# Kernel optimization log

Hardware: AMD Instinct MI355X
Metric: run time of the kernel (lower is better)

Reference implementation:

```python
import jax, jax.numpy as jnp
import numpy as np

D = 1024      # model dimension
H = 16        # heads
DK = D // H   # head dim
DFF = 4096    # ffn hidden
B, S = 2, 2048
EPS = 1e-6
NEG_SLOPE = 0.01  # torch LeakyReLU default


def setup_inputs() -> dict:
    key = jax.random.key(0)
    ks = jax.random.split(key, 12)
    sd = 1.0 / np.sqrt(D)
    sf = 1.0 / np.sqrt(DFF)
    return {
        "x": jax.random.normal(ks[0], (B, S, D), dtype=jnp.float32),
        "wq": jax.random.uniform(ks[1], (D, D), jnp.float32, -sd, sd),
        "bq": jnp.zeros((D,), jnp.float32),
        "wk": jax.random.uniform(ks[2], (D, D), jnp.float32, -sd, sd),
        "bk": jnp.zeros((D,), jnp.float32),
        "wv": jax.random.uniform(ks[3], (D, D), jnp.float32, -sd, sd),
        "bv": jnp.zeros((D,), jnp.float32),
        "wo": jax.random.uniform(ks[4], (D, D), jnp.float32, -sd, sd),
        "bo": jnp.zeros((D,), jnp.float32),
        "g1": jnp.ones((D,), jnp.float32),
        "b1": jnp.zeros((D,), jnp.float32),
        "w_ff1": jax.random.uniform(ks[5], (D, DFF), jnp.float32, -sd, sd),
        "b_ff1": jnp.zeros((DFF,), jnp.float32),
        "w_ff2": jax.random.uniform(ks[6], (DFF, D), jnp.float32, -sf, sf),
        "b_ff2": jnp.zeros((D,), jnp.float32),
        "g2": jnp.ones((D,), jnp.float32),
        "b2": jnp.zeros((D,), jnp.float32),
    }


def _layernorm(x, g, b):
    mu = jnp.mean(x, axis=-1, keepdims=True)
    var = jnp.mean(jnp.square(x - mu), axis=-1, keepdims=True)
    return (x - mu) * jax.lax.rsqrt(var + EPS) * g + b


def reference(x, wq, bq, wk, bk, wv, bv, wo, bo, g1, b1,
              w_ff1, b_ff1, w_ff2, b_ff2, g2, b2):
    # Multi-head attention
    q = (x @ wq + bq).reshape(B, S, H, DK).transpose(0, 2, 1, 3)  # [B,H,S,DK]
    k = (x @ wk + bk).reshape(B, S, H, DK).transpose(0, 2, 1, 3)
    v = (x @ wv + bv).reshape(B, S, H, DK).transpose(0, 2, 1, 3)
    scores = jnp.einsum('bhqd,bhkd->bhqk', q, k) / np.sqrt(DK)
    attn = jax.nn.softmax(scores, axis=-1)
    ctx = jnp.einsum('bhqk,bhkd->bhqd', attn, v)
    ctx = ctx.transpose(0, 2, 1, 3).reshape(B, S, D)
    attn_out = ctx @ wo + bo
    # residual + LN1 (dropout = identity in eval)
    h = _layernorm(attn_out + x, g1, b1)
    # FFN with LeakyReLU
    ff = jnp.where(h @ w_ff1 + b_ff1 > 0,
                   h @ w_ff1 + b_ff1,
                   NEG_SLOPE * (h @ w_ff1 + b_ff1))
    ff = ff @ w_ff2 + b_ff2
    return _layernorm(ff + h, g2, b2)
```

## Files before the change

### kernel.cpp

```cpp
#include <hip/hip_runtime.h>
#include <math.h>

#define D_MODEL 1024
#define NHEAD   16
#define DKH     64
#define DFF_    4096
#define BB      2
#define SS      2048
#define MTOT    (BB*SS)
#define EPSLN   1e-6f
#define NEG_SLOPE 0.01f

typedef unsigned short u16;
typedef unsigned int   u32;
typedef __bf16 bf16x8 __attribute__((ext_vector_type(8)));
typedef float  f32x4  __attribute__((ext_vector_type(4)));
typedef u16    u16x4  __attribute__((ext_vector_type(4)));

__device__ __forceinline__ u16 f2bf(float f) {
    u32 u = __float_as_uint(f);
    u = (u + 0x7fffu + ((u >> 16) & 1u)) >> 16;
    return (u16)u;
}
__device__ __forceinline__ float bf2f(u16 u) {
    return __uint_as_float(((u32)u) << 16);
}

__device__ __forceinline__ void gload_lds16(const u16* g, u16* l) {
    __builtin_amdgcn_global_load_lds(
        (const __attribute__((address_space(1))) u32*)g,
        (__attribute__((address_space(3))) u32*)l,
        16, 0, 0);
}

__device__ __forceinline__ void transpose_tile(const float* __restrict__ W,
        u16* __restrict__ WT, int N, int out_stride, int out_row_off,
        float scale, int bx, int by, u16* T)
{
    const int t  = threadIdx.x;
    const int n0 = bx * 64;
    const int k0 = by * 64;
    #pragma unroll
    for (int i = 0; i < 4; ++i) {
        int r = i * 16 + (t >> 4);
        int c = (t & 15) * 4;
        float4 v = *(const float4*)&W[(size_t)(k0 + r) * N + n0 + c];
        T[(c + 0) * 72 + r] = f2bf(v.x * scale);
        T[(c + 1) * 72 + r] = f2bf(v.y * scale);
        T[(c + 2) * 72 + r] = f2bf(v.z * scale);
        T[(c + 3) * 72 + r] = f2bf(v.w * scale);
    }
    __syncthreads();
    #pragma unroll
    for (int i = 0; i < 4; ++i) {
        int nr = i * 16 + (t >> 4);
        int kc = (t & 15) * 4;
        u16x4 o = { T[nr*72 + kc], T[nr*72 + kc + 1], T[nr*72 + kc + 2], T[nr*72 + kc + 3] };
        *(u16x4*)&WT[(size_t)(out_row_off + n0 + nr) * out_stride + k0 + kc] = o;
    }
}

__global__ __launch_bounds__(256)
void prep(const float* __restrict__ x, u16* __restrict__ x_bf,
          const float* __restrict__ wq, const float* __restrict__ wk,
          const float* __restrict__ wv, const float* __restrict__ wo,
          const float* __restrict__ wff1, const float* __restrict__ wff2,
          u16* __restrict__ wqkvT, u16* __restrict__ woT,
          u16* __restrict__ wff1T, u16* __restrict__ wff2T,
          const float* __restrict__ bq, const float* __restrict__ bk,
          const float* __restrict__ bv, float* __restrict__ qkv_bias,
          float qscale)
{
    __shared__ u16 T[64 * 72];
    int blk = blockIdx.x;
    if (blk < 4096) {
        int i = blk * 256 + threadIdx.x;
        float4 v = ((const float4*)x)[i];
        u16x4 o = { f2bf(v.x), f2bf(v.y), f2bf(v.z), f2bf(v.w) };
        ((u16x4*)x_bf)[i] = o;
        return;
    }
    blk -= 4096;
    if (blk < 1024) {
        int which = blk >> 8, r = blk & 255;
        const float* Ws = which == 0 ? wq : which == 1 ? wk : which == 2 ? wv : wo;
        u16* Wd   = which == 3 ? woT : wqkvT;
        int off   = which == 3 ? 0 : which * 1024;
        float sc  = which == 0 ? qscale : 1.0f;
        transpose_tile(Ws, Wd, 1024, 1024, off, sc, r & 15, r >> 4, T);
        return;
    }
    blk -= 1024;
    if (blk < 1024) {
        transpose_tile(wff1, wff1T, 4096, 1024, 0, 1.0f, blk & 63, blk >> 6, T);
        return;
    }
    blk -= 1024;
    if (blk < 1024) {
        transpose_tile(wff2, wff2T, 1024, 4096, 0, 1.0f, blk & 15, blk >> 4, T);
        return;
    }
    blk -= 1024;
    int i = blk * 256 + threadIdx.x;
    qkv_bias[i] = (i < 1024) ? bq[i] * qscale
                : (i < 2048) ? bk[i - 1024] : bv[i - 2048];
}

template<int EPI>
__global__ __launch_bounds__(256)
void gemm_bf16(const u16* __restrict__ A, const u16* __restrict__ BT,
               const float* __restrict__ bias, void* __restrict__ Cout,
               u16* __restrict__ Vt, int M, int N, int k_len, int kstride)
{
    __shared__ u16 As[128 * 64];
    __shared__ u16 Bs[128 * 64];
    const int tid  = threadIdx.x;
    const int w    = tid >> 6;
    const int lane = tid & 63;
    const int lm   = lane & 15;
    const int lq   = lane >> 4;
    const int nf = gridDim.x * gridDim.y;
    int f = blockIdx.y * gridDim.x + blockIdx.x;
    f = (f & 7) * (nf >> 3) + (f >> 3);
    const int row0 = (f / gridDim.x) * 128;
    const int col0 = (f % gridDim.x) * 128;
    const int k_off = blockIdx.z * k_len;
    const int wrow = (w >> 1) * 64;
    const int wcol = (w & 1) * 64;

    f32x4 acc[4][4] = {};

    const int r_i = lane >> 3;
    const int csw = ((lane & 7) ^ r_i) * 8;
    const u16* a_src = A  + (size_t)(row0 + w * 32 + r_i) * kstride + k_off + csw;
    const u16* b_src = BT + (size_t)(col0 + w * 32 + r_i) * kstride + k_off + csw;
    u16* a_dst = &As[(w * 32) * 64];
    u16* b_dst = &Bs[(w * 32) * 64];

    const int fr0 = (lq ^ (lm & 7)) * 8;
    const int fr1 = ((4 + lq) ^ (lm & 7)) * 8;
    const u16* a_rd = &As[(wrow + lm) * 64];
    const u16* b_rd = &Bs[(wcol + lm) * 64];

    for (int k0 = 0; k0 < k_len; k0 += 64) {
        #pragma unroll
        for (int i = 0; i < 4; ++i) {
            gload_lds16(a_src + k0 + (size_t)(i * 8) * kstride, a_dst + (i * 8) * 64);
            gload_lds16(b_src + k0 + (size_t)(i * 8) * kstride, b_dst + (i * 8) * 64);
        }
        __syncthreads();
        #pragma unroll
        for (int h = 0; h < 2; ++h) {
            const int fo = h ? fr1 : fr0;
            bf16x8 av[4], bv[4];
            #pragma unroll
            for (int m = 0; m < 4; ++m) av[m] = *(const bf16x8*)(a_rd + m * 16 * 64 + fo);
            #pragma unroll
            for (int n = 0; n < 4; ++n) bv[n] = *(const bf16x8*)(b_rd + n * 16 * 64 + fo);
            #pragma unroll
            for (int m = 0; m < 4; ++m)
                #pragma unroll
                for (int n = 0; n < 4; ++n)
                    acc[m][n] = __builtin_amdgcn_mfma_f32_16x16x32_bf16(av[m], bv[n], acc[m][n], 0, 0, 0);
        }
        __syncthreads();
    }

    float bz[4] = {0.f, 0.f, 0.f, 0.f};
    if (EPI != 3) {
        #pragma unroll
        for (int n = 0; n < 4; ++n) bz[n] = bias[col0 + wcol + n * 16 + lm];
    }

    u16* Cz = (u16*)Cout + (EPI == 3 ? (size_t)blockIdx.z * M * N : 0);
    #pragma unroll
    for (int m = 0; m < 4; ++m) {
        #pragma unroll
        for (int e = 0; e < 4; ++e) {
            int row = row0 + wrow + m * 16 + lq * 4 + e;
            #pragma unroll
            for (int n = 0; n < 4; ++n) {
                int col = col0 + wcol + n * 16 + lm;
                float v = acc[m][n][e] + bz[n];
                if (EPI == 1) v = v > 0.f ? v : NEG_SLOPE * v;
                Cz[(size_t)row * N + col] = f2bf(v);
            }
        }
    }
}

#define GPHASE(p) { \
    bf16x8 a0h0 = *(const bf16x8*)&ar[(wm * 128 + (p) * 32 + lm) * 64 + fr0]; \
    bf16x8 a0h1 = *(const bf16x8*)&ar[(wm * 128 + (p) * 32 + lm) * 64 + fr1]; \
    bf16x8 a1h0 = *(const bf16x8*)&ar[(wm * 128 + (p) * 32 + 16 + lm) * 64 + fr0]; \
    bf16x8 a1h1 = *(const bf16x8*)&ar[(wm * 128 + (p) * 32 + 16 + lm) * 64 + fr1]; \
    _Pragma("unroll") \
    for (int n = 0; n < 4; ++n) { \
        acc[2*(p)][n]   = __builtin_amdgcn_mfma_f32_16x16x32_bf16(a0h0, bvf[n][0], acc[2*(p)][n], 0, 0, 0); \
        acc[2*(p)][n]   = __builtin_amdgcn_mfma_f32_16x16x32_bf16(a0h1, bvf[n][1], acc[2*(p)][n], 0, 0, 0); \
        acc[2*(p)+1][n] = __builtin_amdgcn_mfma_f32_16x16x32_bf16(a1h0, bvf[n][0], acc[2*(p)+1][n], 0, 0, 0); \
        acc[2*(p)+1][n] = __builtin_amdgcn_mfma_f32_16x16x32_bf16(a1h1, bvf[n][1], acc[2*(p)+1][n], 0, 0, 0); \
    } }

template<int EPI>
__global__ __launch_bounds__(512, 2)
void gemm256(const u16* __restrict__ A, const u16* __restrict__ BT,
             const float* __restrict__ bias, void* __restrict__ Cout,
             u16* __restrict__ Vt, int M, int N, int k_len, int kstride)
{
    __shared__ u16 AS[2][256 * 64];
    __shared__ u16 BS[2][256 * 64];
    const int tid  = threadIdx.x;
    const int w    = tid >> 6;
    const int lane = tid & 63;
    const int lm   = lane & 15;
    const int lq   = lane >> 4;
    const int wm   = w >> 2;
    const int wn   = w & 3;

    const int gx = gridDim.x;
    const int nf = gx * gridDim.y;
    int f = blockIdx.y * gx + blockIdx.x;
    f = (f & 7) * (nf >> 3) + (f >> 3);
    const int row0 = (f / gx) * 256;
    const int col0 = (f % gx) * 256;

    const int r_i = lane >> 3;
    const int csw = ((lane & 7) ^ r_i) * 8;
    const u16* a_src = A  + (size_t)(row0 + w * 8 + r_i) * kstride + csw;
    const u16* b_src = BT + (size_t)(col0 + w * 8 + r_i) * kstride + csw;

    const int fr0 = (lq ^ (lm & 7)) * 8;
    const int fr1 = ((4 + lq) ^ (lm & 7)) * 8;

    f32x4 acc[8][4] = {};
    const int NT = k_len >> 6;

    #pragma unroll
    for (int j = 0; j < 4; ++j) {
        gload_lds16(a_src + (size_t)(j * 64) * kstride, &AS[0][(j * 64 + w * 8) * 64]);
        gload_lds16(b_src + (size_t)(j * 64) * kstride, &BS[0][(j * 64 + w * 8) * 64]);
    }
    __syncthreads();

    for (int kt = 0; kt < NT; ++kt) {
        const int cb = kt & 1, nb = cb ^ 1;
        const bool pre = (kt + 1) < NT;
        const u16* ar = &AS[cb][0];
        const u16* br = &BS[cb][0];
        u16* aw = &AS[nb][0];
        u16* bw = &BS[nb][0];
        const size_t knext = (size_t)(kt + 1) * 64;

        if (pre) {
            #pragma unroll
            for (int j = 0; j < 4; ++j)
                gload_lds16(b_src + (size_t)(j * 64) * kstride + knext,
                            bw + (j * 64 + w * 8) * 64);
            asm volatile("s_waitcnt vmcnt(6)" ::: "memory");
        } else {
            asm volatile("s_waitcnt vmcnt(2)" ::: "memory");
        }
        bf16x8 bvf[4][2];
        #pragma unroll
        for (int n = 0; n < 4; ++n) {
            bvf[n][0] = *(const bf16x8*)&br[(wn * 64 + n * 16 + lm) * 64 + fr0];
            bvf[n][1] = *(const bf16x8*)&br[(wn * 64 + n * 16 + lm) * 64 + fr1];
        }
        GPHASE(0)
        if (pre) {
            gload_lds16(a_src + knext,                                 aw + (w * 8) * 64);
            gload_lds16(a_src + (size_t)128 * kstride + knext,         aw + (128 + w * 8) * 64);
        }
        GPHASE(1)
        if (pre) {
            gload_lds16(a_src + (size_t)64 * kstride + knext,          aw + (64 + w * 8) * 64);
            gload_lds16(a_src + (size_t)192 * kstride + knext,         aw + (192 + w * 8) * 64);
            asm volatile("s_waitcnt vmcnt(8)" ::: "memory");
        } else {
            asm volatile("s_waitcnt vmcnt(0)" ::: "memory");
        }
        GPHASE(2)
        GPHASE(3)
        asm volatile("" ::: "memory");
        __builtin_amdgcn_s_barrier();
    }

    float bz[4];
    #pragma unroll
    for (int n = 0; n < 4; ++n) bz[n] = bias[col0 + wn * 64 + n * 16 + lm];

    if (EPI == 4 && col0 >= 2048) {
        #pragma unroll
        for (int m = 0; m < 8; ++m) {
            int rbase = row0 + wm * 128 + m * 16 + lq * 4;
            int b = rbase >> 11, s = rbase & 2047;
            #pragma unroll
            for (int n = 0; n < 4; ++n) {
                int c = col0 + wn * 64 + n * 16 + lm - 2048;
                u16x4 pk = { f2bf(acc[m][n][0] + bz[n]), f2bf(acc[m][n][1] + bz[n]),
                             f2bf(acc[m][n][2] + bz[n]), f2bf(acc[m][n][3] + bz[n]) };
                *(u16x4*)&Vt[(size_t)((b * 16 + (c >> 6)) * 64 + (c & 63)) * 2048 + s] = pk;
            }
        }
        return;
    }

    u16* Cz = (u16*)Cout;
    #pragma unroll
    for (int m = 0; m < 8; ++m) {
        #pragma unroll
        for (int e = 0; e < 4; ++e) {
            int row = row0 + wm * 128 + m * 16 + lq * 4 + e;
            #pragma unroll
            for (int n = 0; n < 4; ++n) {
                int col = col0 + wn * 64 + n * 16 + lm;
                float v = acc[m][n][e] + bz[n];
                if (EPI == 1) v = v > 0.f ? v : NEG_SLOPE * v;
                Cz[(size_t)row * N + col] = f2bf(v);
            }
        }
    }
}

__global__ __launch_bounds__(256, 4)
void attn_mfma(const u16* __restrict__ QKV, const u16* __restrict__ Vt,
               u16* __restrict__ ctx)
{
    __shared__ u16 QP[64 * 64];
    __shared__ u16 Kb[2][64 * 64];
    __shared__ u16 Vb[2][64 * 64];
    const int tid = threadIdx.x, w = tid >> 6, lane = tid & 63;
    const int lm = lane & 15, lq = lane >> 4;
    const int qh = w >> 1;
    const int kh = w & 1;
    int f = blockIdx.y * 32 + blockIdx.x;
    f = (f & 7) * 128 + (f >> 3);
    const int q0 = (f & 31) * 64;
    const int bh = f >> 5;
    const int b  = bh >> 4, h = bh & 15;
    const size_t row_b = (size_t)b * SS;
    const int ccol = h * DKH;

    const int r_i = lane >> 3;
    const int csw = ((lane & 7) ^ r_i) * 8;
    const u16* ksrc = QKV + (row_b + w * 16 + r_i) * 3072 + 1024 + ccol + csw;
    const u16* vsrc = Vt + ((size_t)bh * 64 + w * 16 + r_i) * SS + csw;
    const u16* qsrc = QKV + (row_b + q0 + w * 16 + r_i) * 3072 + ccol + csw;

    gload_lds16(qsrc,                    &QP[(w * 16) * 64]);
    gload_lds16(qsrc + (size_t)8 * 3072, &QP[(w * 16 + 8) * 64]);
    #pragma unroll
    for (int i = 0; i < 2; ++i) {
        gload_lds16(ksrc + (size_t)(i * 8) * 3072, &Kb[0][(w * 16 + i * 8) * 64]);
        gload_lds16(vsrc + (size_t)(i * 8) * SS,   &Vb[0][(w * 16 + i * 8) * 64]);
    }
    __syncthreads();

    const int fr0 = (lq ^ (lm & 7)) * 8;
    const int fr1 = ((4 + lq) ^ (lm & 7)) * 8;
    const int frp = kh ? fr1 : fr0;

    bf16x8 aq[2][2];
    #pragma unroll
    for (int m = 0; m < 2; ++m) {
        aq[m][0] = *(const bf16x8*)&QP[(qh * 32 + m * 16 + lm) * 64 + fr0];
        aq[m][1] = *(const bf16x8*)&QP[(qh * 32 + m * 16 + lm) * 64 + fr1];
    }
    __syncthreads();

    bf16x8 ones;
    #pragma unroll
    for (int j = 0; j < 8; ++j) ones[j] = (__bf16)1.0f;

    f32x4 o[2][4] = {};
    f32x4 lacc[2] = {};

    for (int kt = 0; kt < SS / 64; ++kt) {
        const int cur = kt & 1;
        if (kt < SS / 64 - 1) {
            const int nxt = cur ^ 1;
            const size_t koff = (size_t)(kt + 1) * 64;
            #pragma unroll
            for (int i = 0; i < 2; ++i) {
                gload_lds16(ksrc + (koff + i * 8) * 3072, &Kb[nxt][(w * 16 + i * 8) * 64]);
                gload_lds16(vsrc + koff + (size_t)(i * 8) * SS, &Vb[nxt][(w * 16 + i * 8) * 64]);
            }
        }
        f32x4 s[2][2] = {};
        #pragma unroll
        for (int n = 0; n < 2; ++n) {
            bf16x8 bk0 = *(const bf16x8*)&Kb[cur][(kh * 32 + n * 16 + lm) * 64 + fr0];
            bf16x8 bk1 = *(const bf16x8*)&Kb[cur][(kh * 32 + n * 16 + lm) * 64 + fr1];
            #pragma unroll
            for (int m = 0; m < 2; ++m) {
                s[m][n] = __builtin_amdgcn_mfma_f32_16x16x32_bf16(aq[m][0], bk0, s[m][n], 0, 0, 0);
                s[m][n] = __builtin_amdgcn_mfma_f32_16x16x32_bf16(aq[m][1], bk1, s[m][n], 0, 0, 0);
            }
        }
        const int rb = lq * 4;
        const int cw = lm & 7;
        #pragma unroll
        for (int m = 0; m < 2; ++m) {
            #pragma unroll
            for (int n = 0; n < 2; ++n) {
                const int cb = kh * 4 + n * 2 + (lm >> 3);
                #pragma unroll
                for (int e = 0; e < 4; ++e) {
                    float p = __builtin_exp2f(s[m][n][e]);
                    const int row = qh * 32 + m * 16 + rb + e;
                    QP[row * 64 + ((cb ^ ((rb + e) & 7)) * 8) + cw] =
                        (u16)((__float_as_uint(p) + 0x8000u) >> 16);
                }
            }
        }
        bf16x8 ap[2];
        #pragma unroll
        for (int m = 0; m < 2; ++m)
            ap[m] = *(const bf16x8*)&QP[(qh * 32 + m * 16 + lm) * 64 + frp];
        #pragma unroll
        for (int n = 0; n < 4; ++n) {
            bf16x8 bv = *(const bf16x8*)&Vb[cur][(n * 16 + lm) * 64 + frp];
            #pragma unroll
            for (int m = 0; m < 2; ++m)
                o[m][n] = __builtin_amdgcn_mfma_f32_16x16x32_bf16(ap[m], bv, o[m][n], 0, 0, 0);
        }
        #pragma unroll
        for (int m = 0; m < 2; ++m)
            lacc[m] = __builtin_amdgcn_mfma_f32_16x16x32_bf16(ap[m], ones, lacc[m], 0, 0, 0);
        __syncthreads();
    }

    if (kh == 1) {
        float* red = (float*)(qh == 0 ? (void*)Kb : (void*)Vb);
        #pragma unroll
        for (int m = 0; m < 2; ++m) {
            #pragma unroll
            for (int n = 0; n < 4; ++n)
                #pragma unroll
                for (int e = 0; e < 4; ++e)
                    red[((m * 4 + n) * 4 + e) * 64 + lane] = o[m][n][e];
            #pragma unroll
            for (int e = 0; e < 4; ++e)
                red[(32 + m * 4 + e) * 64 + lane] = lacc[m][e];
        }
    }
    __syncthreads();
    if (kh == 0) {
        const float* red = (const float*)(qh == 0 ? (void*)Kb : (void*)Vb);
        #pragma unroll
        for (int m = 0; m < 2; ++m) {
            #pragma unroll
            for (int e = 0; e < 4; ++e)
                lacc[m][e] += red[(32 + m * 4 + e) * 64 + lane];
            #pragma unroll
            for (int e = 0; e < 4; ++e) {
                float inv = 1.0f / lacc[m][e];
                int row = q0 + qh * 32 + m * 16 + lq * 4 + e;
                u16* dst = ctx + (row_b + row) * D_MODEL + ccol;
                #pragma unroll
                for (int n = 0; n < 4; ++n) {
                    float v = o[m][n][e] + red[((m * 4 + n) * 4 + e) * 64 + lane];
                    dst[n * 16 + lm] = f2bf(v * inv);
                }
            }
        }
    }
}

template<int OUTF32, int RESBF>
__global__ __launch_bounds__(256)
void add_ln(const u16* __restrict__ C0, const u16* __restrict__ C1,
            const float* __restrict__ cbias, const void* __restrict__ resid,
            const float* __restrict__ g, const float* __restrict__ beta,
            float* __restrict__ outf, u16* __restrict__ outb)
{
    __shared__ float red[8];
    const int row = blockIdx.x;
    const int tid = threadIdx.x;
    u16x4 p0 = ((const u16x4*)(C0 + (size_t)row * D_MODEL))[tid];
    u16x4 p1 = ((const u16x4*)(C1 + (size_t)row * D_MODEL))[tid];
    float4 cb = ((const float4*)cbias)[tid];
    float4 rr;
    if (RESBF) {
        u16x4 rb = ((const u16x4*)((const u16*)resid + (size_t)row * D_MODEL))[tid];
        rr = { bf2f(rb.x), bf2f(rb.y), bf2f(rb.z), bf2f(rb.w) };
    } else {
        rr = ((const float4*)((const float*)resid + (size_t)row * D_MODEL))[tid];
    }
    float4 v = { bf2f(p0.x) + bf2f(p1.x) + cb.x + rr.x,
                 bf2f(p0.y) + bf2f(p1.y) + cb.y + rr.y,
                 bf2f(p0.z) + bf2f(p1.z) + cb.z + rr.z,
                 bf2f(p0.w) + bf2f(p1.w) + cb.w + rr.w };
    float s  = v.x + v.y + v.z + v.w;
    float sq = v.x*v.x + v.y*v.y + v.z*v.z + v.w*v.w;
    #pragma unroll
    for (int off = 32; off > 0; off >>= 1) {
        s  += __shfl_down(s,  off, 64);
        sq += __shfl_down(sq, off, 64);
    }
    const int wv = tid >> 6;
    if ((tid & 63) == 0) { red[wv] = s; red[4 + wv] = sq; }
    __syncthreads();
    float st  = red[0] + red[1] + red[2] + red[3];
    float sqt = red[4] + red[5] + red[6] + red[7];
    float mu   = st * (1.0f / D_MODEL);
    float var  = sqt * (1.0f / D_MODEL) - mu * mu;
    float rstd = rsqrtf(var + EPSLN);
    float4 gv = ((const float4*)g)[tid];
    float4 bt = ((const float4*)beta)[tid];
    float4 ov;
    ov.x = (v.x - mu) * rstd * gv.x + bt.x;
    ov.y = (v.y - mu) * rstd * gv.y + bt.y;
    ov.z = (v.z - mu) * rstd * gv.z + bt.z;
    ov.w = (v.w - mu) * rstd * gv.w + bt.w;
    if (OUTF32) {
        ((float4*)(outf + (size_t)row * D_MODEL))[tid] = ov;
    } else {
        u16x4 ob = { f2bf(ov.x), f2bf(ov.y), f2bf(ov.z), f2bf(ov.w) };
        ((u16x4*)(outb + (size_t)row * D_MODEL))[tid] = ob;
    }
}

extern "C" void kernel_launch(void* const* d_in, const int* in_sizes, int n_in,
                              void* d_out, int out_size, void* d_ws, size_t ws_size,
                              hipStream_t stream) {
    const float* x     = (const float*)d_in[0];
    const float* wq    = (const float*)d_in[1];
    const float* bq    = (const float*)d_in[2];
    const float* wk    = (const float*)d_in[3];
    const float* bk    = (const float*)d_in[4];
    const float* wv    = (const float*)d_in[5];
    const float* bv    = (const float*)d_in[6];
    const float* wo    = (const float*)d_in[7];
    const float* bo    = (const float*)d_in[8];
    const float* g1    = (const float*)d_in[9];
    const float* b1    = (const float*)d_in[10];
    const float* w_ff1 = (const float*)d_in[11];
    const float* b_ff1 = (const float*)d_in[12];
    const float* w_ff2 = (const float*)d_in[13];
    const float* b_ff2 = (const float*)d_in[14];
    const float* g2    = (const float*)d_in[15];
    const float* b2    = (const float*)d_in[16];
    float* out = (float*)d_out;

    const float qscale = 0.18033688011112042f;

    char* W = (char*)d_ws;
    u16*   x_bf    = (u16*)(W + 0);
    u16*   wqkvT   = (u16*)(W + 8388608);
    u16*   woT     = (u16*)(W + 14680064);
    u16*   wff1T   = (u16*)(W + 16777216);
    u16*   wff2T   = (u16*)(W + 25165824);
    u16*   QKV     = (u16*)(W + 33554432);
    u16*   VtG     = (u16*)(W + 58720256);
    u16*   C0      = (u16*)(W + 67108864);
    u16*   C1      = (u16*)(W + 75497472);
    u16*   h_bf    = (u16*)(W + 83886080);
    float* qkv_bias= (float*)(W + 92274688);
    u16*   ctx     = x_bf;
    u16*   ff1_bf  = QKV;

    dim3 blk(256);
    dim3 blk5(512);
    prep<<<7180, blk, 0, stream>>>(x, x_bf, wq, wk, wv, wo, w_ff1, w_ff2,
                                   wqkvT, woT, wff1T, wff2T,
                                   bq, bk, bv, qkv_bias, qscale);
    gemm256<4><<<dim3(12, 16, 1), blk5, 0, stream>>>(x_bf, wqkvT, qkv_bias, QKV, VtG, MTOT, 3072, 1024, 1024);
    attn_mfma<<<dim3(32, 32), blk, 0, stream>>>(QKV, VtG, ctx);
    gemm_bf16<3><<<dim3(8, 32, 2), blk, 0, stream>>>(ctx, woT, nullptr, C0, nullptr, MTOT, 1024, 512, 1024);
    add_ln<0, 0><<<MTOT, blk, 0, stream>>>(C0, C1, bo, x, g1, b1, nullptr, h_bf);
    gemm256<1><<<dim3(16, 16, 1), blk5, 0, stream>>>(h_bf, wff1T, b_ff1, ff1_bf, nullptr, MTOT, DFF_, 1024, 1024);
    gemm_bf16<3><<<dim3(8, 32, 2), blk, 0, stream>>>(ff1_bf, wff2T, nullptr, C0, nullptr, MTOT, 1024, 2048, 4096);
    add_ln<1, 1><<<MTOT, blk, 0, stream>>>(C0, C1, b_ff2, h_bf, g2, b2, out, nullptr);
}
```

Measured before the change: 350.8 us.

## Move FF2 to 256-tile split-K GEMM and add barrier-synced MFMA phases with setprio

The FF2 projection moves from the 128-tile gemm_bf16 with split-K 2 to the 256-tile gemm256 kernel with split-K 4. The four partial outputs go to C0 and to the now-free x_bf buffer, and add_ln gains a four-partial reduction path. gemm256's inner loop is restructured so each A-fragment phase is loaded, fenced by s_barrier, and run under raised s_setprio. This keeps the waves in lockstep and is meant to interleave LDS reads with MFMA issue. The trade-offs are more partial-sum traffic, many extra barriers per K step, and reuse of x_bf as scratch.

```diff
diff --git a/kernel.cpp b/kernel.cpp
--- a/kernel.cpp
+++ b/kernel.cpp
@@ -32,6 +32,8 @@
         (__attribute__((address_space(3))) u32*)l,
         16, 0, 0);
 }
+
+#define MF(a, b, c) __builtin_amdgcn_mfma_f32_16x16x32_bf16(a, b, c, 0, 0, 0)
 
 __device__ __forceinline__ void transpose_tile(const float* __restrict__ W,
         u16* __restrict__ WT, int N, int out_stride, int out_row_off,
@@ -161,7 +163,7 @@
             for (int m = 0; m < 4; ++m)
                 #pragma unroll
                 for (int n = 0; n < 4; ++n)
-                    acc[m][n] = __builtin_amdgcn_mfma_f32_16x16x32_bf16(av[m], bv[n], acc[m][n], 0, 0, 0);
+                    acc[m][n] = MF(av[m], bv[n], acc[m][n]);
         }
         __syncthreads();
     }
@@ -189,18 +191,16 @@
     }
 }
 
-#define GPHASE(p) { \
-    bf16x8 a0h0 = *(const bf16x8*)&ar[(wm * 128 + (p) * 32 + lm) * 64 + fr0]; \
-    bf16x8 a0h1 = *(const bf16x8*)&ar[(wm * 128 + (p) * 32 + lm) * 64 + fr1]; \
-    bf16x8 a1h0 = *(const bf16x8*)&ar[(wm * 128 + (p) * 32 + 16 + lm) * 64 + fr0]; \
-    bf16x8 a1h1 = *(const bf16x8*)&ar[(wm * 128 + (p) * 32 + 16 + lm) * 64 + fr1]; \
+#define MPHASE(p) \
+    __builtin_amdgcn_s_setprio(1); \
     _Pragma("unroll") \
     for (int n = 0; n < 4; ++n) { \
-        acc[2*(p)][n]   = __builtin_amdgcn_mfma_f32_16x16x32_bf16(a0h0, bvf[n][0], acc[2*(p)][n], 0, 0, 0); \
-        acc[2*(p)][n]   = __builtin_amdgcn_mfma_f32_16x16x32_bf16(a0h1, bvf[n][1], acc[2*(p)][n], 0, 0, 0); \
-        acc[2*(p)+1][n] = __builtin_amdgcn_mfma_f32_16x16x32_bf16(a1h0, bvf[n][0], acc[2*(p)+1][n], 0, 0, 0); \
-        acc[2*(p)+1][n] = __builtin_amdgcn_mfma_f32_16x16x32_bf16(a1h1, bvf[n][1], acc[2*(p)+1][n], 0, 0, 0); \
-    } }
+        acc[2*(p)][n]   = MF(a00, bvf[n][0], acc[2*(p)][n]); \
+        acc[2*(p)][n]   = MF(a01, bvf[n][1], acc[2*(p)][n]); \
+        acc[2*(p)+1][n] = MF(a10, bvf[n][0], acc[2*(p)+1][n]); \
+        acc[2*(p)+1][n] = MF(a11, bvf[n][1], acc[2*(p)+1][n]); \
+    } \
+    __builtin_amdgcn_s_setprio(0);
 
 template<int EPI>
 __global__ __launch_bounds__(512, 2)
@@ -224,11 +224,12 @@
     f = (f & 7) * (nf >> 3) + (f >> 3);
     const int row0 = (f / gx) * 256;
     const int col0 = (f % gx) * 256;
+    const int k_off = blockIdx.z * k_len;
 
     const int r_i = lane >> 3;
     const int csw = ((lane & 7) ^ r_i) * 8;
-    const u16* a_src = A  + (size_t)(row0 + w * 8 + r_i) * kstride + csw;
-    const u16* b_src = BT + (size_t)(col0 + w * 8 + r_i) * kstride + csw;
+    const u16* a_src = A  + (size_t)(row0 + w * 8 + r_i) * kstride + k_off + csw;
+    const u16* b_src = BT + (size_t)(col0 + w * 8 + r_i) * kstride + k_off + csw;
 
     const int fr0 = (lq ^ (lm & 7)) * 8;
     const int fr1 = ((4 + lq) ^ (lm & 7)) * 8;
@@ -267,28 +268,60 @@
             bvf[n][0] = *(const bf16x8*)&br[(wn * 64 + n * 16 + lm) * 64 + fr0];
             bvf[n][1] = *(const bf16x8*)&br[(wn * 64 + n * 16 + lm) * 64 + fr1];
         }
-        GPHASE(0)
+        bf16x8 a00 = *(const bf16x8*)&ar[(wm * 128 + lm) * 64 + fr0];
+        bf16x8 a01 = *(const bf16x8*)&ar[(wm * 128 + lm) * 64 + fr1];
+        bf16x8 a10 = *(const bf16x8*)&ar[(wm * 128 + 16 + lm) * 64 + fr0];
+        bf16x8 a11 = *(const bf16x8*)&ar[(wm * 128 + 16 + lm) * 64 + fr1];
+        asm volatile("s_waitcnt lgkmcnt(8)" ::: "memory");
+        __builtin_amdgcn_s_barrier();
+        asm volatile("s_waitcnt lgkmcnt(0)" ::: "memory");
+        MPHASE(0)
+        __builtin_amdgcn_s_barrier();
+
         if (pre) {
-            gload_lds16(a_src + knext,                                 aw + (w * 8) * 64);
-            gload_lds16(a_src + (size_t)128 * kstride + knext,         aw + (128 + w * 8) * 64);
-        }
-        GPHASE(1)
+            gload_lds16(a_src + knext,                         aw + (w * 8) * 64);
+            gload_lds16(a_src + (size_t)128 * kstride + knext, aw + (128 + w * 8) * 64);
+        }
+        a00 = *(const bf16x8*)&ar[(wm * 128 + 32 + lm) * 64 + fr0];
+        a01 = *(const bf16x8*)&ar[(wm * 128 + 32 + lm) * 64 + fr1];
+        a10 = *(const bf16x8*)&ar[(wm * 128 + 48 + lm) * 64 + fr0];
+        a11 = *(const bf16x8*)&ar[(wm * 128 + 48 + lm) * 64 + fr1];
+        __builtin_amdgcn_s_barrier();
+        asm volatile("s_waitcnt lgkmcnt(0)" ::: "memory");
+        MPHASE(1)
+        __builtin_amdgcn_s_barrier();
+
         if (pre) {
-            gload_lds16(a_src + (size_t)64 * kstride + knext,          aw + (64 + w * 8) * 64);
-            gload_lds16(a_src + (size_t)192 * kstride + knext,         aw + (192 + w * 8) * 64);
+            gload_lds16(a_src + (size_t)64 * kstride + knext,  aw + (64 + w * 8) * 64);
+            gload_lds16(a_src + (size_t)192 * kstride + knext, aw + (192 + w * 8) * 64);
             asm volatile("s_waitcnt vmcnt(8)" ::: "memory");
         } else {
             asm volatile("s_waitcnt vmcnt(0)" ::: "memory");
         }
-        GPHASE(2)
-        GPHASE(3)
-        asm volatile("" ::: "memory");
-        __builtin_amdgcn_s_barrier();
-    }
-
-    float bz[4];
-    #pragma unroll
-    for (int n = 0; n < 4; ++n) bz[n] = bias[col0 + wn * 64 + n * 16 + lm];
+        a00 = *(const bf16x8*)&ar[(wm * 128 + 64 + lm) * 64 + fr0];
+        a01 = *(const bf16x8*)&ar[(wm * 128 + 64 + lm) * 64 + fr1];
+        a10 = *(const bf16x8*)&ar[(wm * 128 + 80 + lm) * 64 + fr0];
+        a11 = *(const bf16x8*)&ar[(wm * 128 + 80 + lm) * 64 + fr1];
+        __builtin_amdgcn_s_barrier();
+        asm volatile("s_waitcnt lgkmcnt(0)" ::: "memory");
+        MPHASE(2)
+        __builtin_amdgcn_s_barrier();
+
+        a00 = *(const bf16x8*)&ar[(wm * 128 + 96 + lm) * 64 + fr0];
+        a01 = *(const bf16x8*)&ar[(wm * 128 + 96 + lm) * 64 + fr1];
+        a10 = *(const bf16x8*)&ar[(wm * 128 + 112 + lm) * 64 + fr0];
+        a11 = *(const bf16x8*)&ar[(wm * 128 + 112 + lm) * 64 + fr1];
+        __builtin_amdgcn_s_barrier();
+        asm volatile("s_waitcnt lgkmcnt(0)" ::: "memory");
+        MPHASE(3)
+        __builtin_amdgcn_s_barrier();
+    }
+
+    float bz[4] = {0.f, 0.f, 0.f, 0.f};
+    if (EPI != 3) {
+        #pragma unroll
+        for (int n = 0; n < 4; ++n) bz[n] = bias[col0 + wn * 64 + n * 16 + lm];
+    }
 
     if (EPI == 4 && col0 >= 2048) {
         #pragma unroll
@@ -306,7 +339,14 @@
         return;
     }
 
-    u16* Cz = (u16*)Cout;
+    u16* Cz;
+    if (EPI == 3) {
+        const size_t ps = (size_t)M * N;
+        Cz = (blockIdx.z < 2) ? (u16*)Cout + blockIdx.z * ps
+                              : Vt + (blockIdx.z - 2) * ps;
+    } else {
+        Cz = (u16*)Cout;
+    }
     #pragma unroll
     for (int m = 0; m < 8; ++m) {
         #pragma unroll
@@ -394,8 +434,8 @@
             bf16x8 bk1 = *(const bf16x8*)&Kb[cur][(kh * 32 + n * 16 + lm) * 64 + fr1];
             #pragma unroll
             for (int m = 0; m < 2; ++m) {
-                s[m][n] = __builtin_amdgcn_mfma_f32_16x16x32_bf16(aq[m][0], bk0, s[m][n], 0, 0, 0);
-                s[m][n] = __builtin_amdgcn_mfma_f32_16x16x32_bf16(aq[m][1], bk1, s[m][n], 0, 0, 0);
+                s[m][n] = MF(aq[m][0], bk0, s[m][n]);
+                s[m][n] = MF(aq[m][1], bk1, s[m][n]);
             }
         }
         const int rb = lq * 4;
@@ -423,11 +463,11 @@
             bf16x8 bv = *(const bf16x8*)&Vb[cur][(n * 16 + lm) * 64 + frp];
             #pragma unroll
             for (int m = 0; m < 2; ++m)
-                o[m][n] = __builtin_amdgcn_mfma_f32_16x16x32_bf16(ap[m], bv, o[m][n], 0, 0, 0);
+                o[m][n] = MF(ap[m], bv, o[m][n]);
         }
         #pragma unroll
         for (int m = 0; m < 2; ++m)
-            lacc[m] = __builtin_amdgcn_mfma_f32_16x16x32_bf16(ap[m], ones, lacc[m], 0, 0, 0);
+            lacc[m] = MF(ap[m], ones, lacc[m]);
         __syncthreads();
     }
 
@@ -468,7 +508,7 @@
     }
 }
 
-template<int OUTF32, int RESBF>
+template<int OUTF32, int RESBF, int NPART>
 __global__ __launch_bounds__(256)
 void add_ln(const u16* __restrict__ C0, const u16* __restrict__ C1,
             const float* __restrict__ cbias, const void* __restrict__ resid,
@@ -478,8 +518,23 @@
     __shared__ float red[8];
     const int row = blockIdx.x;
     const int tid = threadIdx.x;
-    u16x4 p0 = ((const u16x4*)(C0 + (size_t)row * D_MODEL))[tid];
-    u16x4 p1 = ((const u16x4*)(C1 + (size_t)row * D_MODEL))[tid];
+    float4 pv;
+    if (NPART == 2) {
+        u16x4 p0 = ((const u16x4*)(C0 + (size_t)row * D_MODEL))[tid];
+        u16x4 p1 = ((const u16x4*)(C1 + (size_t)row * D_MODEL))[tid];
+        pv = { bf2f(p0.x) + bf2f(p1.x), bf2f(p0.y) + bf2f(p1.y),
+               bf2f(p0.z) + bf2f(p1.z), bf2f(p0.w) + bf2f(p1.w) };
+    } else {
+        const size_t ps = (size_t)MTOT * D_MODEL;
+        u16x4 p0 = ((const u16x4*)(C0 + (size_t)row * D_MODEL))[tid];
+        u16x4 p1 = ((const u16x4*)(C0 + ps + (size_t)row * D_MODEL))[tid];
+        u16x4 p2 = ((const u16x4*)(C1 + (size_t)row * D_MODEL))[tid];
+        u16x4 p3 = ((const u16x4*)(C1 + ps + (size_t)row * D_MODEL))[tid];
+        pv.x = (bf2f(p0.x) + bf2f(p1.x)) + (bf2f(p2.x) + bf2f(p3.x));
+        pv.y = (bf2f(p0.y) + bf2f(p1.y)) + (bf2f(p2.y) + bf2f(p3.y));
+        pv.z = (bf2f(p0.z) + bf2f(p1.z)) + (bf2f(p2.z) + bf2f(p3.z));
+        pv.w = (bf2f(p0.w) + bf2f(p1.w)) + (bf2f(p2.w) + bf2f(p3.w));
+    }
     float4 cb = ((const float4*)cbias)[tid];
     float4 rr;
     if (RESBF) {
@@ -488,10 +543,8 @@
     } else {
         rr = ((const float4*)((const float*)resid + (size_t)row * D_MODEL))[tid];
     }
-    float4 v = { bf2f(p0.x) + bf2f(p1.x) + cb.x + rr.x,
-                 bf2f(p0.y) + bf2f(p1.y) + cb.y + rr.y,
-                 bf2f(p0.z) + bf2f(p1.z) + cb.z + rr.z,
-                 bf2f(p0.w) + bf2f(p1.w) + cb.w + rr.w };
+    float4 v = { pv.x + cb.x + rr.x, pv.y + cb.y + rr.y,
+                 pv.z + cb.z + rr.z, pv.w + cb.w + rr.w };
     float s  = v.x + v.y + v.z + v.w;
     float sq = v.x*v.x + v.y*v.y + v.z*v.z + v.w*v.w;
     #pragma unroll
@@ -569,8 +622,8 @@
     gemm256<4><<<dim3(12, 16, 1), blk5, 0, stream>>>(x_bf, wqkvT, qkv_bias, QKV, VtG, MTOT, 3072, 1024, 1024);
     attn_mfma<<<dim3(32, 32), blk, 0, stream>>>(QKV, VtG, ctx);
     gemm_bf16<3><<<dim3(8, 32, 2), blk, 0, stream>>>(ctx, woT, nullptr, C0, nullptr, MTOT, 1024, 512, 1024);
-    add_ln<0, 0><<<MTOT, blk, 0, stream>>>(C0, C1, bo, x, g1, b1, nullptr, h_bf);
+    add_ln<0, 0, 2><<<MTOT, blk, 0, stream>>>(C0, C1, bo, x, g1, b1, nullptr, h_bf);
     gemm256<1><<<dim3(16, 16, 1), blk5, 0, stream>>>(h_bf, wff1T, b_ff1, ff1_bf, nullptr, MTOT, DFF_, 1024, 1024);
-    gemm_bf16<3><<<dim3(8, 32, 2), blk, 0, stream>>>(ff1_bf, wff2T, nullptr, C0, nullptr, MTOT, 1024, 2048, 4096);
-    add_ln<1, 1><<<MTOT, blk, 0, stream>>>(C0, C1, b_ff2, h_bf, g2, b2, out, nullptr);
-}
+    gemm256<3><<<dim3(4, 16, 4), blk5, 0, stream>>>(ff1_bf, wff2T, nullptr, C0, x_bf, MTOT, 1024, 1024, 4096);
+    add_ln<1, 1, 4><<<MTOT, blk, 0, stream>>>(C0, x_bf, b_ff2, h_bf, g2, b2, out, nullptr);
+}
```

Measured after the change: 381.8 us. 1.09x slower.
